# Optimization experiments

Measured on AMD Instinct MI355X. Metric: run time of the kernel, lower is better.

Reference implementation:

```python
import jax, jax.numpy as jnp
import numpy as np

V, R, A, C, T = 10000, 5, 8, 64, 64
EPS = 1e-3  # keras BatchNormalization default epsilon


def setup_inputs() -> dict:
    key = jax.random.key(0)
    ks = jax.random.split(key, 8)
    signal = jax.random.normal(ks[0], (V, C), dtype=jnp.float32)
    bc_idx = jax.random.randint(ks[1], (V, R, A, 3), 0, V, dtype=jnp.int32)
    bc_w = jax.random.uniform(ks[2], (V, R, A, 3), dtype=jnp.float32)
    bc_w = bc_w / jnp.sum(bc_w, axis=-1, keepdims=True)  # barycentric weights sum to 1
    scale = 0.05
    templates1 = jax.random.normal(ks[3], (T, R, A, C), dtype=jnp.float32) * scale
    bias1 = jax.random.normal(ks[4], (T,), dtype=jnp.float32) * scale
    templates2 = jax.random.normal(ks[5], (T, R, A, T), dtype=jnp.float32) * scale
    bias2 = jax.random.normal(ks[6], (T,), dtype=jnp.float32) * scale
    return {
        "signal": signal,
        "bc_w": bc_w,
        "templates1": templates1,
        "bias1": bias1,
        "gamma1": jnp.ones((T,), jnp.float32),
        "beta1": jnp.zeros((T,), jnp.float32),
        "templates2": templates2,
        "bias2": bias2,
        "gamma2": jnp.ones((T,), jnp.float32),
        "beta2": jnp.zeros((T,), jnp.float32),
        "bc_idx": bc_idx,
    }


def _conv_dirac(sig, bc_idx, bc_w, templates, bias):
    # Barycentric interpolation (the 'patch operator'): gather 3 mesh-vertex
    # signals per template point and blend. gathered: (V, R, A, 3, Cin)
    gathered = sig[bc_idx]
    interp = jnp.einsum("vraic,vrai->vrac", gathered, bc_w)  # (V, R, A, Cin)
    # All A rotations of the template along the angular axis:
    # rolled signal[a] = interp[(a - o) % A]  <=>  contract with templates[(a + o) % A].
    rot = (jnp.arange(A)[:, None] + jnp.arange(A)[None, :]) % A  # (O, A)
    t_rot = templates[:, :, rot, :]  # (T, R, O, A, Cin)
    return jnp.einsum("vrac,troac->vot", interp, t_rot) + bias  # (V, O, T)


def _angular_max_pool(x):
    # Pick, per vertex, the rotation with maximal Euclidean response norm.
    idx = jnp.argmax(jnp.linalg.norm(x, axis=-1), axis=1)  # (V,)
    return jnp.take_along_axis(x, idx[:, None, None], axis=1)[:, 0, :]  # (V, T)


def _bn_inference(x, gamma, beta):
    # Fresh BN at inference: moving_mean = 0, moving_var = 1.
    inv = jax.lax.rsqrt(jnp.asarray(1.0 + EPS, x.dtype))
    return gamma * (x * inv) + beta


def reference(signal, bc_w, templates1, bias1, gamma1, beta1,
              templates2, bias2, gamma2, beta2, bc_idx):
    s = _conv_dirac(signal, bc_idx, bc_w, templates1, bias1)
    s = jax.nn.relu(_bn_inference(_angular_max_pool(s), gamma1, beta1))
    s = _conv_dirac(s, bc_idx, bc_w, templates2, bias2)
    s = _bn_inference(_angular_max_pool(s), gamma2, beta2)
    # input_dim == amt_templates -> identity shortcut (no rescale branch)
    return jax.nn.relu(s + signal)
```

## Files before the change

### kernel.cpp

```cpp
#include <hip/hip_runtime.h>

#define NVV 10000
#define NKSTEPS 80
#define BN_INV 0.99950037468777316f

#define AS1 __attribute__((address_space(1)))
#define AS3 __attribute__((address_space(3)))

typedef float f32x4 __attribute__((ext_vector_type(4)));
typedef short short8 __attribute__((ext_vector_type(8)));
typedef unsigned short ushort;

#define ACH_USH 5120
#define ACH_B   10240
#define WCH_B   16384

__device__ __forceinline__ ushort bsplit(float v, float& rem) {
    unsigned u = __float_as_uint(v);
    unsigned r = (u + 0x7fffu + ((u >> 16) & 1u)) & 0xffff0000u;
    rem = v - __uint_as_float(r);
    return (ushort)(r >> 16);
}

__device__ __forceinline__ void interp_store2(ushort* __restrict__ dstp, int it,
                                              const float4& g0, const float4& g1, const float4& g2,
                                              float w0, float w1, float w2) {
    const int m = it >> 3, kq = it & 7;
    const float av[4] = {g0.x, g0.y, g0.z, g0.w};
    const float bv[4] = {g1.x, g1.y, g1.z, g1.w};
    const float cv[4] = {g2.x, g2.y, g2.z, g2.w};
    ushort h1[4], h2[4];
    #pragma unroll
    for (int e = 0; e < 4; ++e) {
        const float vv = w0 * av[e] + w1 * bv[e] + w2 * cv[e];
        float r1, r2;
        h1[e] = bsplit(vv, r1); h2[e] = bsplit(r1, r2);
    }
    const int mt = m >> 4, mm = m & 15, qk = kq >> 1, hf = kq & 1;
    const int o0 = ((mt * 2 + 0) * 4 + qk) * 128 + mm * 8 + hf * 4;
    *(uint2*)(dstp + o0)       = make_uint2((unsigned)h1[0] | ((unsigned)h1[1] << 16),
                                            (unsigned)h1[2] | ((unsigned)h1[3] << 16));
    *(uint2*)(dstp + o0 + 512) = make_uint2((unsigned)h2[0] | ((unsigned)h2[1] << 16),
                                            (unsigned)h2[2] | ((unsigned)h2[3] << 16));
}

__global__ void build_w_kernel(const float* __restrict__ t1,
                               const float* __restrict__ t2,
                               ushort* __restrict__ W1g,
                               ushort* __restrict__ W2g) {
    const int k = blockIdx.x;
    const int n = threadIdx.x;
    const float* T  = blockIdx.y ? t2 : t1;
    ushort*      Wg = blockIdx.y ? W2g : W1g;
    const int r = k >> 9, a = (k >> 6) & 7, c = k & 63;
    const int o = n >> 6, t = n & 63;
    const float w = T[((t * 5 + r) * 8 + ((o + a) & 7)) * 64 + c];
    float r1, r2;
    const ushort h1 = bsplit(w, r1);
    const ushort h2 = bsplit(r1, r2);
    const int kstep = k >> 5, kw = k & 31, q = kw >> 3, kk = kw & 7;
    const int strip = n >> 7, nl = n & 127, nt = nl >> 4, l16 = nl & 15;
    const size_t base = (size_t)(kstep * 4 + strip) * 8192;
    const int off = ((nt * 2 + 0) * 4 + q) * 128 + l16 * 8 + kk;
    Wg[base + off]       = h1;
    Wg[base + off + 512] = h2;
}

__global__ void interp_kernel(const float* __restrict__ src,
                              const int*   __restrict__ bc_idx,
                              const float* __restrict__ bc_w,
                              ushort*      __restrict__ Ag,
                              int mg0) {
    const int cid = blockIdx.x;
    const int mgl = cid / NKSTEPS;
    const int ks  = cid % NKSTEPS;
    const int mg  = mg0 + mgl;
    const int x   = threadIdx.x;
    ushort* chunk = Ag + (size_t)cid * ACH_USH;
    const int ra = ks >> 1;
    #pragma unroll
    for (int s = 0; s < 3; ++s) {
        const int it = x + 256 * s;
        if (it < 640) {
            const int m = it >> 3, kq = it & 7;
            const int v = mg * 80 + m;
            const int*   ip = bc_idx + v * 120 + ra * 3;
            const float* wp = bc_w  + v * 120 + ra * 3;
            const int c0 = (ks & 1) * 32 + kq * 4;
            const float4 g0 = *(const float4*)(src + (size_t)ip[0] * 64 + c0);
            const float4 g1 = *(const float4*)(src + (size_t)ip[1] * 64 + c0);
            const float4 g2 = *(const float4*)(src + (size_t)ip[2] * 64 + c0);
            interp_store2(chunk, it, g0, g1, g2, wp[0], wp[1], wp[2]);
        }
    }
}

__global__ __launch_bounds__(256, 3)
void gemm_kernel(const ushort* __restrict__ Ag,
                 const ushort* __restrict__ Wg,
                 const float* __restrict__ bias,
                 float*       __restrict__ S,
                 float*       __restrict__ normsq,
                 int mg0, int Pp, int mpx) {
    __shared__ ushort sW[2][8192];
    __shared__ ushort sA[2][ACH_USH];
    const int x = threadIdx.x;
    const int b = blockIdx.x;
    const int xcd  = b & 7;
    const int rest = b >> 3;
    const int strip = rest & 3;
    const int mgl_l = rest >> 2;
    const int mg_local = xcd * mpx + mgl_l;
    if (mg_local >= Pp) return;
    const int mg    = mg0 + mg_local;
    const int Mbase = mg * 80;
    const int wj  = x >> 6;
    const int l16 = x & 15;
    const int q   = (x & 63) >> 4;

    f32x4 d[5][2] = {};

    const char* gWb = (const char*)Wg;
    const char* gAb = (const char*)Ag + (size_t)mg_local * NKSTEPS * ACH_B;

    {
        const char* gw = gWb + (size_t)(0 * 4 + strip) * WCH_B;
        char*       lw = (char*)sW[0];
        #pragma unroll
        for (int j = 0; j < 4; ++j)
            __builtin_amdgcn_global_load_lds((AS1 const void*)(gw + (x + 256 * j) * 16),
                                             (AS3 void*)(lw + (x + 256 * j) * 16), 16, 0, 0);
        const char* ga = gAb;
        char*       la = (char*)sA[0];
        #pragma unroll
        for (int j = 0; j < 3; ++j) {
            const int it = x + 256 * j;
            if (it < 640)
                __builtin_amdgcn_global_load_lds((AS1 const void*)(ga + it * 16),
                                                 (AS3 void*)(la + it * 16), 16, 0, 0);
        }
    }
    __syncthreads();

    for (int ks = 0; ks < NKSTEPS; ++ks) {
        const int cur = ks & 1, nxt = cur ^ 1;
        if (ks + 1 < NKSTEPS) {
            const char* gw = gWb + (size_t)((ks + 1) * 4 + strip) * WCH_B;
            char*       lw = (char*)sW[nxt];
            #pragma unroll
            for (int j = 0; j < 4; ++j)
                __builtin_amdgcn_global_load_lds((AS1 const void*)(gw + (x + 256 * j) * 16),
                                                 (AS3 void*)(lw + (x + 256 * j) * 16), 16, 0, 0);
            const char* ga = gAb + (size_t)(ks + 1) * ACH_B;
            char*       la = (char*)sA[nxt];
            #pragma unroll
            for (int j = 0; j < 3; ++j) {
                const int it = x + 256 * j;
                if (it < 640)
                    __builtin_amdgcn_global_load_lds((AS1 const void*)(ga + it * 16),
                                                     (AS3 void*)(la + it * 16), 16, 0, 0);
            }
        }

        short8 w1f[2], w2f[2];
        #pragma unroll
        for (int nt = 0; nt < 2; ++nt) {
            const int ntg = 2 * wj + nt;
            w1f[nt] = *(const short8*)(sW[cur] + ((ntg * 2 + 0) * 4 + q) * 128 + l16 * 8);
            w2f[nt] = *(const short8*)(sW[cur] + ((ntg * 2 + 1) * 4 + q) * 128 + l16 * 8);
        }
        #pragma unroll
        for (int mt = 0; mt < 5; ++mt) {
            const short8 a1 = *(const short8*)(sA[cur] + ((mt * 2 + 0) * 4 + q) * 128 + l16 * 8);
            const short8 a2 = *(const short8*)(sA[cur] + ((mt * 2 + 1) * 4 + q) * 128 + l16 * 8);
            #pragma unroll
            for (int nt = 0; nt < 2; ++nt) {
                d[mt][nt] = __builtin_amdgcn_mfma_f32_16x16x32_bf16(a1, w1f[nt], d[mt][nt], 0, 0, 0);
                d[mt][nt] = __builtin_amdgcn_mfma_f32_16x16x32_bf16(a1, w2f[nt], d[mt][nt], 0, 0, 0);
                d[mt][nt] = __builtin_amdgcn_mfma_f32_16x16x32_bf16(a2, w1f[nt], d[mt][nt], 0, 0, 0);
            }
        }
        __syncthreads();
    }

    float* sN = (float*)sA;
    float bs[2];
    #pragma unroll
    for (int nt = 0; nt < 2; ++nt)
        bs[nt] = bias[(32 * wj + 16 * nt + l16) & 63];

    float p[5][4];
    #pragma unroll
    for (int mt = 0; mt < 5; ++mt)
        #pragma unroll
        for (int r = 0; r < 4; ++r) p[mt][r] = 0.0f;

    #pragma unroll
    for (int mt = 0; mt < 5; ++mt) {
        #pragma unroll
        for (int nt = 0; nt < 2; ++nt) {
            #pragma unroll
            for (int r = 0; r < 4; ++r) {
                const float val = d[mt][nt][r] + bs[nt];
                const int mglob = Mbase + mt * 16 + q * 4 + r;
                const int nglob = strip * 128 + wj * 32 + nt * 16 + l16;
                S[(size_t)mglob * 512 + nglob] = val;
                p[mt][r] += val * val;
            }
        }
    }
    #pragma unroll
    for (int mt = 0; mt < 5; ++mt)
        #pragma unroll
        for (int r = 0; r < 4; ++r) {
            float v = p[mt][r];
            v += __shfl_xor(v, 1, 64);
            v += __shfl_xor(v, 2, 64);
            v += __shfl_xor(v, 4, 64);
            v += __shfl_xor(v, 8, 64);
            p[mt][r] = v;
        }
    if (l16 == 0) {
        #pragma unroll
        for (int mt = 0; mt < 5; ++mt)
            #pragma unroll
            for (int r = 0; r < 4; ++r)
                sN[wj * 80 + mt * 16 + q * 4 + r] = p[mt][r];
    }
    __syncthreads();
    if (x < 80) {
        const int v = Mbase + x;
        normsq[(size_t)v * 8 + strip * 2]     = sN[0 * 80 + x] + sN[1 * 80 + x];
        normsq[(size_t)v * 8 + strip * 2 + 1] = sN[2 * 80 + x] + sN[3 * 80 + x];
    }
}

template<bool RES>
__global__ void pool_kernel(const float* __restrict__ S,
                            const float* __restrict__ normsq,
                            const float* __restrict__ gamma,
                            const float* __restrict__ beta,
                            const float* __restrict__ resid,
                            float*       __restrict__ dst) {
    const int gid = blockIdx.x * 256 + threadIdx.x;
    const int v = gid >> 6, t = gid & 63;
    const float* nv = normsq + (size_t)v * 8;
    float bv = nv[0];
    int   bj = 0;
    #pragma unroll
    for (int j = 1; j < 8; ++j) {
        const float tv = nv[j];
        if (tv > bv) { bv = tv; bj = j; }
    }
    const float val = S[(size_t)v * 512 + bj * 64 + t];
    float r = gamma[t] * (val * BN_INV) + beta[t];
    if (RES) r += resid[(size_t)v * 64 + t];
    dst[(size_t)v * 64 + t] = fmaxf(r, 0.0f);
}

extern "C" void kernel_launch(void* const* d_in, const int* in_sizes, int n_in,
                              void* d_out, int out_size, void* d_ws, size_t ws_size,
                              hipStream_t stream) {
    const float* signal = (const float*)d_in[0];
    const float* bc_w   = (const float*)d_in[1];
    const float* t1     = (const float*)d_in[2];
    const float* bias1  = (const float*)d_in[3];
    const float* gamma1 = (const float*)d_in[4];
    const float* beta1  = (const float*)d_in[5];
    const float* t2     = (const float*)d_in[6];
    const float* bias2  = (const float*)d_in[7];
    const float* gamma2 = (const float*)d_in[8];
    const float* beta2  = (const float*)d_in[9];
    const int*   bc_idx = (const int*)d_in[10];

    const size_t WSTG = (size_t)NKSTEPS * 4 * 8192;
    ushort* W1g = (ushort*)d_ws;
    ushort* W2g = W1g + WSTG;
    float* S      = (float*)(W2g + WSTG);
    float* normsq = S + (size_t)NVV * 512;
    float* s1     = normsq + (size_t)NVV * 8;
    ushort* Ag    = (ushort*)(s1 + (size_t)NVV * 64);
    float* out    = (float*)d_out;

    const size_t used  = (size_t)((char*)Ag - (char*)d_ws);
    const size_t avail = ws_size > used ? ws_size - used : 0;
    int P = (int)(avail / ((size_t)NKSTEPS * ACH_B));
    if (P > 125) P = 125;
    if (P < 1)  P = 1;

    build_w_kernel<<<dim3(2560, 2), 512, 0, stream>>>(t1, t2, W1g, W2g);

    for (int mg0 = 0; mg0 < 125; mg0 += P) {
        const int Pp  = (125 - mg0 < P) ? (125 - mg0) : P;
        const int mpx = (Pp + 7) / 8;
        interp_kernel<<<Pp * NKSTEPS, 256, 0, stream>>>(signal, bc_idx, bc_w, Ag, mg0);
        gemm_kernel<<<32 * mpx, 256, 0, stream>>>(Ag, W1g, bias1, S, normsq, mg0, Pp, mpx);
    }
    pool_kernel<false><<<2500, 256, 0, stream>>>(S, normsq, gamma1, beta1, nullptr, s1);

    for (int mg0 = 0; mg0 < 125; mg0 += P) {
        const int Pp  = (125 - mg0 < P) ? (125 - mg0) : P;
        const int mpx = (Pp + 7) / 8;
        interp_kernel<<<Pp * NKSTEPS, 256, 0, stream>>>(s1, bc_idx, bc_w, Ag, mg0);
        gemm_kernel<<<32 * mpx, 256, 0, stream>>>(Ag, W2g, bias2, S, normsq, mg0, Pp, mpx);
    }
    pool_kernel<true><<<2500, 256, 0, stream>>>(S, normsq, gamma2, beta2, signal, out);
}
```

Before: 322.4 us.

## Split GEMM K dimension in two and move bias/norm reduction into pool

Each GEMM block now handles half of the K steps, doubling the grid, and writes raw partial sums into one of two buffers. The pool kernel sums the two partials, adds the bias, and computes per-rotation norms with wave shuffles before the argmax. This aims to raise GPU occupancy and cut per-block latency in the GEMM, at the cost of an extra full-size intermediate buffer, doubled write/read traffic and less workspace for the staged A chunks.

Result: slower. 359.0 us (+11.4%).

```diff
diff --git a/kernel.cpp b/kernel.cpp
--- a/kernel.cpp
+++ b/kernel.cpp
@@ -2,6 +2,7 @@
 
 #define NVV 10000
 #define NKSTEPS 80
+#define KSPLIT 40
 #define BN_INV 0.99950037468777316f
 
 #define AS1 __attribute__((address_space(1)))
@@ -98,22 +99,23 @@
 __global__ __launch_bounds__(256, 3)
 void gemm_kernel(const ushort* __restrict__ Ag,
                  const ushort* __restrict__ Wg,
-                 const float* __restrict__ bias,
-                 float*       __restrict__ S,
-                 float*       __restrict__ normsq,
+                 float*       __restrict__ S1,
+                 float*       __restrict__ S2,
                  int mg0, int Pp, int mpx) {
     __shared__ ushort sW[2][8192];
     __shared__ ushort sA[2][ACH_USH];
     const int x = threadIdx.x;
     const int b = blockIdx.x;
-    const int xcd  = b & 7;
-    const int rest = b >> 3;
-    const int strip = rest & 3;
-    const int mgl_l = rest >> 2;
+    const int xcd   = b & 7;
+    const int rest  = b >> 3;
+    const int khalf = rest & 1;
+    const int strip = (rest >> 1) & 3;
+    const int mgl_l = rest >> 3;
     const int mg_local = xcd * mpx + mgl_l;
     if (mg_local >= Pp) return;
     const int mg    = mg0 + mg_local;
     const int Mbase = mg * 80;
+    const int ks0   = khalf * KSPLIT;
     const int wj  = x >> 6;
     const int l16 = x & 15;
     const int q   = (x & 63) >> 4;
@@ -124,13 +126,13 @@
     const char* gAb = (const char*)Ag + (size_t)mg_local * NKSTEPS * ACH_B;
 
     {
-        const char* gw = gWb + (size_t)(0 * 4 + strip) * WCH_B;
+        const char* gw = gWb + (size_t)(ks0 * 4 + strip) * WCH_B;
         char*       lw = (char*)sW[0];
         #pragma unroll
         for (int j = 0; j < 4; ++j)
             __builtin_amdgcn_global_load_lds((AS1 const void*)(gw + (x + 256 * j) * 16),
                                              (AS3 void*)(lw + (x + 256 * j) * 16), 16, 0, 0);
-        const char* ga = gAb;
+        const char* ga = gAb + (size_t)ks0 * ACH_B;
         char*       la = (char*)sA[0];
         #pragma unroll
         for (int j = 0; j < 3; ++j) {
@@ -142,9 +144,10 @@
     }
     __syncthreads();
 
-    for (int ks = 0; ks < NKSTEPS; ++ks) {
-        const int cur = ks & 1, nxt = cur ^ 1;
-        if (ks + 1 < NKSTEPS) {
+    for (int ki = 0; ki < KSPLIT; ++ki) {
+        const int ks = ks0 + ki;
+        const int cur = ki & 1, nxt = cur ^ 1;
+        if (ki + 1 < KSPLIT) {
             const char* gw = gWb + (size_t)((ks + 1) * 4 + strip) * WCH_B;
             char*       lw = (char*)sW[nxt];
             #pragma unroll
@@ -183,76 +186,52 @@
         __syncthreads();
     }
 
-    float* sN = (float*)sA;
-    float bs[2];
-    #pragma unroll
-    for (int nt = 0; nt < 2; ++nt)
-        bs[nt] = bias[(32 * wj + 16 * nt + l16) & 63];
-
-    float p[5][4];
-    #pragma unroll
-    for (int mt = 0; mt < 5; ++mt)
-        #pragma unroll
-        for (int r = 0; r < 4; ++r) p[mt][r] = 0.0f;
-
+    float* Sh = khalf ? S2 : S1;
     #pragma unroll
     for (int mt = 0; mt < 5; ++mt) {
         #pragma unroll
         for (int nt = 0; nt < 2; ++nt) {
             #pragma unroll
             for (int r = 0; r < 4; ++r) {
-                const float val = d[mt][nt][r] + bs[nt];
                 const int mglob = Mbase + mt * 16 + q * 4 + r;
                 const int nglob = strip * 128 + wj * 32 + nt * 16 + l16;
-                S[(size_t)mglob * 512 + nglob] = val;
-                p[mt][r] += val * val;
+                Sh[(size_t)mglob * 512 + nglob] = d[mt][nt][r];
             }
         }
     }
-    #pragma unroll
-    for (int mt = 0; mt < 5; ++mt)
-        #pragma unroll
-        for (int r = 0; r < 4; ++r) {
-            float v = p[mt][r];
-            v += __shfl_xor(v, 1, 64);
-            v += __shfl_xor(v, 2, 64);
-            v += __shfl_xor(v, 4, 64);
-            v += __shfl_xor(v, 8, 64);
-            p[mt][r] = v;
-        }
-    if (l16 == 0) {
-        #pragma unroll
-        for (int mt = 0; mt < 5; ++mt)
-            #pragma unroll
-            for (int r = 0; r < 4; ++r)
-                sN[wj * 80 + mt * 16 + q * 4 + r] = p[mt][r];
-    }
-    __syncthreads();
-    if (x < 80) {
-        const int v = Mbase + x;
-        normsq[(size_t)v * 8 + strip * 2]     = sN[0 * 80 + x] + sN[1 * 80 + x];
-        normsq[(size_t)v * 8 + strip * 2 + 1] = sN[2 * 80 + x] + sN[3 * 80 + x];
-    }
 }
 
 template<bool RES>
-__global__ void pool_kernel(const float* __restrict__ S,
-                            const float* __restrict__ normsq,
+__global__ void pool_kernel(const float* __restrict__ S1,
+                            const float* __restrict__ S2,
+                            const float* __restrict__ bias,
                             const float* __restrict__ gamma,
                             const float* __restrict__ beta,
                             const float* __restrict__ resid,
                             float*       __restrict__ dst) {
-    const int gid = blockIdx.x * 256 + threadIdx.x;
-    const int v = gid >> 6, t = gid & 63;
-    const float* nv = normsq + (size_t)v * 8;
-    float bv = nv[0];
-    int   bj = 0;
+    const int w = threadIdx.x >> 6;
+    const int t = threadIdx.x & 63;
+    const int v = blockIdx.x * 4 + w;
+    const float bt = bias[t];
+    float vals[8], n2[8];
+    #pragma unroll
+    for (int o = 0; o < 8; ++o) {
+        const size_t idx = (size_t)v * 512 + o * 64 + t;
+        const float val = S1[idx] + S2[idx] + bt;
+        vals[o] = val;
+        float s = val * val;
+        #pragma unroll
+        for (int off = 1; off < 64; off <<= 1) s += __shfl_xor(s, off, 64);
+        n2[o] = s;
+    }
+    int bj = 0; float bv = n2[0];
     #pragma unroll
     for (int j = 1; j < 8; ++j) {
-        const float tv = nv[j];
-        if (tv > bv) { bv = tv; bj = j; }
-    }
-    const float val = S[(size_t)v * 512 + bj * 64 + t];
+        if (n2[j] > bv) { bv = n2[j]; bj = j; }
+    }
+    float val = vals[0];
+    #pragma unroll
+    for (int j = 1; j < 8; ++j) val = (bj == j) ? vals[j] : val;
     float r = gamma[t] * (val * BN_INV) + beta[t];
     if (RES) r += resid[(size_t)v * 64 + t];
     dst[(size_t)v * 64 + t] = fmaxf(r, 0.0f);
@@ -276,11 +255,11 @@
     const size_t WSTG = (size_t)NKSTEPS * 4 * 8192;
     ushort* W1g = (ushort*)d_ws;
     ushort* W2g = W1g + WSTG;
-    float* S      = (float*)(W2g + WSTG);
-    float* normsq = S + (size_t)NVV * 512;
-    float* s1     = normsq + (size_t)NVV * 8;
-    ushort* Ag    = (ushort*)(s1 + (size_t)NVV * 64);
-    float* out    = (float*)d_out;
+    float* S1 = (float*)(W2g + WSTG);
+    float* S2 = S1 + (size_t)NVV * 512;
+    float* s1 = S2 + (size_t)NVV * 512;
+    ushort* Ag = (ushort*)(s1 + (size_t)NVV * 64);
+    float* out = (float*)d_out;
 
     const size_t used  = (size_t)((char*)Ag - (char*)d_ws);
     const size_t avail = ws_size > used ? ws_size - used : 0;
@@ -294,15 +273,15 @@
         const int Pp  = (125 - mg0 < P) ? (125 - mg0) : P;
         const int mpx = (Pp + 7) / 8;
         interp_kernel<<<Pp * NKSTEPS, 256, 0, stream>>>(signal, bc_idx, bc_w, Ag, mg0);
-        gemm_kernel<<<32 * mpx, 256, 0, stream>>>(Ag, W1g, bias1, S, normsq, mg0, Pp, mpx);
-    }
-    pool_kernel<false><<<2500, 256, 0, stream>>>(S, normsq, gamma1, beta1, nullptr, s1);
+        gemm_kernel<<<64 * mpx, 256, 0, stream>>>(Ag, W1g, S1, S2, mg0, Pp, mpx);
+    }
+    pool_kernel<false><<<2500, 256, 0, stream>>>(S1, S2, bias1, gamma1, beta1, nullptr, s1);
 
     for (int mg0 = 0; mg0 < 125; mg0 += P) {
         const int Pp  = (125 - mg0 < P) ? (125 - mg0) : P;
         const int mpx = (Pp + 7) / 8;
         interp_kernel<<<Pp * NKSTEPS, 256, 0, stream>>>(s1, bc_idx, bc_w, Ag, mg0);
-        gemm_kernel<<<32 * mpx, 256, 0, stream>>>(Ag, W2g, bias2, S, normsq, mg0, Pp, mpx);
-    }
-    pool_kernel<true><<<2500, 256, 0, stream>>>(S, normsq, gamma2, beta2, signal, out);
-}
+        gemm_kernel<<<64 * mpx, 256, 0, stream>>>(Ag, W2g, S1, S2, mg0, Pp, mpx);
+    }
+    pool_kernel<true><<<2500, 256, 0, stream>>>(S1, S2, bias2, gamma2, beta2, signal, out);
+}
```

## Load GEMM fragments directly from global into registers, dropping LDS staging

Applied to the files above, without the earlier changes.

The GEMM main loop stops staging A and W chunks through double-buffered LDS with global_load_lds and per-step barriers. Each wave now loads its MFMA operand fragments straight from global memory into registers, double-buffered across two k-steps, so no __syncthreads is needed inside the loop. LDS shrinks to a small norm-reduction buffer, and launch bounds drop from 3 to 2 waves per SIMD to make room for the larger register footprint. The risk is that A fragments are read redundantly by all four waves from global/L2 instead of once per block, and lower occupancy gives less latency hiding.

Result: slower. 333.3 us (+3.4%).

```diff
diff --git a/kernel.cpp b/kernel.cpp
--- a/kernel.cpp
+++ b/kernel.cpp
@@ -95,15 +95,40 @@
     }
 }
 
-__global__ __launch_bounds__(256, 3)
+#define GEMM_LOADS(AB, WB, KS)                                              \
+    if ((KS) < NKSTEPS) {                                                   \
+        const AS1 char* an = aBase + (size_t)(KS) * ACH_B;                  \
+        const AS1 char* wn = wBase + (size_t)(KS) * (4 * WCH_B);            \
+        _Pragma("unroll")                                                   \
+        for (int f = 0; f < 10; ++f)                                        \
+            AB[f] = *(const AS1 short8*)(an + f * 1024);                    \
+        _Pragma("unroll")                                                   \
+        for (int f = 0; f < 4; ++f)                                         \
+            WB[f] = *(const AS1 short8*)(wn + f * 1024);                    \
+    }
+
+#define GEMM_MFMAS(AB, WB)                                                  \
+    _Pragma("unroll")                                                       \
+    for (int mt = 0; mt < 5; ++mt) {                                        \
+        _Pragma("unroll")                                                   \
+        for (int nt = 0; nt < 2; ++nt) {                                    \
+            d[mt][nt] = __builtin_amdgcn_mfma_f32_16x16x32_bf16(            \
+                AB[mt * 2 + 0], WB[nt * 2 + 0], d[mt][nt], 0, 0, 0);        \
+            d[mt][nt] = __builtin_amdgcn_mfma_f32_16x16x32_bf16(            \
+                AB[mt * 2 + 0], WB[nt * 2 + 1], d[mt][nt], 0, 0, 0);        \
+            d[mt][nt] = __builtin_amdgcn_mfma_f32_16x16x32_bf16(            \
+                AB[mt * 2 + 1], WB[nt * 2 + 0], d[mt][nt], 0, 0, 0);        \
+        }                                                                   \
+    }
+
+__global__ __launch_bounds__(256, 2)
 void gemm_kernel(const ushort* __restrict__ Ag,
                  const ushort* __restrict__ Wg,
                  const float* __restrict__ bias,
                  float*       __restrict__ S,
                  float*       __restrict__ normsq,
                  int mg0, int Pp, int mpx) {
-    __shared__ ushort sW[2][8192];
-    __shared__ ushort sA[2][ACH_USH];
+    __shared__ float sN[4 * 80];
     const int x = threadIdx.x;
     const int b = blockIdx.x;
     const int xcd  = b & 7;
@@ -114,76 +139,29 @@
     if (mg_local >= Pp) return;
     const int mg    = mg0 + mg_local;
     const int Mbase = mg * 80;
-    const int wj  = x >> 6;
-    const int l16 = x & 15;
-    const int q   = (x & 63) >> 4;
+    const int wj   = x >> 6;
+    const int lane = x & 63;
+    const int l16  = lane & 15;
+    const int q    = lane >> 4;
 
     f32x4 d[5][2] = {};
 
-    const char* gWb = (const char*)Wg;
-    const char* gAb = (const char*)Ag + (size_t)mg_local * NKSTEPS * ACH_B;
-
-    {
-        const char* gw = gWb + (size_t)(0 * 4 + strip) * WCH_B;
-        char*       lw = (char*)sW[0];
-        #pragma unroll
-        for (int j = 0; j < 4; ++j)
-            __builtin_amdgcn_global_load_lds((AS1 const void*)(gw + (x + 256 * j) * 16),
-                                             (AS3 void*)(lw + (x + 256 * j) * 16), 16, 0, 0);
-        const char* ga = gAb;
-        char*       la = (char*)sA[0];
-        #pragma unroll
-        for (int j = 0; j < 3; ++j) {
-            const int it = x + 256 * j;
-            if (it < 640)
-                __builtin_amdgcn_global_load_lds((AS1 const void*)(ga + it * 16),
-                                                 (AS3 void*)(la + it * 16), 16, 0, 0);
-        }
-    }
-    __syncthreads();
-
-    for (int ks = 0; ks < NKSTEPS; ++ks) {
-        const int cur = ks & 1, nxt = cur ^ 1;
-        if (ks + 1 < NKSTEPS) {
-            const char* gw = gWb + (size_t)((ks + 1) * 4 + strip) * WCH_B;
-            char*       lw = (char*)sW[nxt];
-            #pragma unroll
-            for (int j = 0; j < 4; ++j)
-                __builtin_amdgcn_global_load_lds((AS1 const void*)(gw + (x + 256 * j) * 16),
-                                                 (AS3 void*)(lw + (x + 256 * j) * 16), 16, 0, 0);
-            const char* ga = gAb + (size_t)(ks + 1) * ACH_B;
-            char*       la = (char*)sA[nxt];
-            #pragma unroll
-            for (int j = 0; j < 3; ++j) {
-                const int it = x + 256 * j;
-                if (it < 640)
-                    __builtin_amdgcn_global_load_lds((AS1 const void*)(ga + it * 16),
-                                                     (AS3 void*)(la + it * 16), 16, 0, 0);
-            }
-        }
-
-        short8 w1f[2], w2f[2];
-        #pragma unroll
-        for (int nt = 0; nt < 2; ++nt) {
-            const int ntg = 2 * wj + nt;
-            w1f[nt] = *(const short8*)(sW[cur] + ((ntg * 2 + 0) * 4 + q) * 128 + l16 * 8);
-            w2f[nt] = *(const short8*)(sW[cur] + ((ntg * 2 + 1) * 4 + q) * 128 + l16 * 8);
-        }
-        #pragma unroll
-        for (int mt = 0; mt < 5; ++mt) {
-            const short8 a1 = *(const short8*)(sA[cur] + ((mt * 2 + 0) * 4 + q) * 128 + l16 * 8);
-            const short8 a2 = *(const short8*)(sA[cur] + ((mt * 2 + 1) * 4 + q) * 128 + l16 * 8);
-            #pragma unroll
-            for (int nt = 0; nt < 2; ++nt) {
-                d[mt][nt] = __builtin_amdgcn_mfma_f32_16x16x32_bf16(a1, w1f[nt], d[mt][nt], 0, 0, 0);
-                d[mt][nt] = __builtin_amdgcn_mfma_f32_16x16x32_bf16(a1, w2f[nt], d[mt][nt], 0, 0, 0);
-                d[mt][nt] = __builtin_amdgcn_mfma_f32_16x16x32_bf16(a2, w1f[nt], d[mt][nt], 0, 0, 0);
-            }
-        }
-        __syncthreads();
-    }
-
-    float* sN = (float*)sA;
+    const AS1 char* aBase = (const AS1 char*)Ag
+        + (size_t)mg_local * NKSTEPS * ACH_B + lane * 16;
+    const AS1 char* wBase = (const AS1 char*)Wg
+        + (size_t)strip * WCH_B + (size_t)wj * 4096 + lane * 16;
+
+    short8 A0[10], W0[4], A1[10], W1[4];
+
+    GEMM_LOADS(A0, W0, 0);
+
+    for (int ks2 = 0; ks2 < NKSTEPS; ks2 += 2) {
+        GEMM_LOADS(A1, W1, ks2 + 1);
+        GEMM_MFMAS(A0, W0);
+        GEMM_LOADS(A0, W0, ks2 + 2);
+        GEMM_MFMAS(A1, W1);
+    }
+
     float bs[2];
     #pragma unroll
     for (int nt = 0; nt < 2; ++nt)
```
